# Optimization experiments

Measured on AMD Instinct MI355X. Metric: run time of the kernel, lower is better.

The kernel has to match this reference:

```python
import jax, jax.numpy as jnp
import numpy as np

NUM_EMBEDDINGS = 8192
EMBEDDING_DIM = 256
COMMITMENT_COST = 0.25


def setup_inputs() -> dict:
    key = jax.random.key(0)
    k1, k2 = jax.random.split(key)
    inputs = jax.random.normal(k1, (64, 512, EMBEDDING_DIM), dtype=jnp.float32)
    # nn.Embedding weight initialized uniform(-0.1, 0.1)
    emb_w = jax.random.uniform(k2, (NUM_EMBEDDINGS, EMBEDDING_DIM), dtype=jnp.float32,
                               minval=-0.1, maxval=0.1)
    return {"inputs": inputs, "emb_w": emb_w}


def reference(inputs, emb_w):
    x = jnp.clip(inputs, -1.0, 1.0)
    flat = x.reshape(-1, EMBEDDING_DIM)                      # [N, D]
    distances = (jnp.sum(flat * flat, axis=1, keepdims=True)
                 + jnp.sum(emb_w * emb_w, axis=1)
                 - 2.0 * jnp.einsum('nd,kd->nk', flat, emb_w))
    encoding_indices = jnp.argmin(distances, axis=1)         # [N]
    quantized = emb_w[encoding_indices].reshape(x.shape)     # [B, T, D]
    # loss = mse(stop_grad(q), x) + beta * mse(q, stop_grad(x))
    loss = (jnp.mean((jax.lax.stop_gradient(quantized) - x) ** 2)
            + COMMITMENT_COST * jnp.mean((quantized - jax.lax.stop_gradient(x)) ** 2))
    # straight-through estimator
    quantized_st = x + jax.lax.stop_gradient(quantized - x)
    return (quantized_st, loss)
```

## Files before the change

### kernel.cpp

```cpp
#include <hip/hip_runtime.h>


#define D        256
#define KCODES   8192
#define NROWS    32768
#define MB       64
#define SLOTS    128
#define THREADS  512
#define CAP      32
#define MARGIN   0.03f
#define BIAS     32.0f
#define NOUT     8388608

typedef _Float16 h8_t __attribute__((ext_vector_type(8)));
typedef float    f4_t __attribute__((ext_vector_type(4)));

__device__ __forceinline__ float clipf(float v) { return fminf(1.0f, fmaxf(-1.0f, v)); }

#define DPP_ROR(x, n) __int_as_float(__builtin_amdgcn_update_dpp( \
    0, __float_as_int(x), 0x120 + (n), 0xF, 0xF, true))
__device__ __forceinline__ float maxrow16(float x) {
  x = fmaxf(x, DPP_ROR(x, 1));
  x = fmaxf(x, DPP_ROR(x, 2));
  x = fmaxf(x, DPP_ROR(x, 4));
  x = fmaxf(x, DPP_ROR(x, 8));
  return x;
}

__global__ void vq_packsetup(const float* __restrict__ emb, _Float16* __restrict__ femb,
                             float* __restrict__ senp, float* __restrict__ ekkb,
                             float* __restrict__ lossacc) {
  const int t = blockIdx.x;
  if (t == 0 && threadIdx.x == 0) lossacc[0] = 0.0f;
  #pragma unroll
  for (int j = 0; j < 4; ++j) {
    int g = t * 1024 + j * 256 + threadIdx.x;
    int ch = g >> 9, u = g & 511;
    int kc = u >> 6, ln = u & 63;
    int code = ch * 16 + (ln & 15);
    int k0 = kc * 32 + (ln >> 4) * 8;
    const float* sp = emb + (size_t)code * D + k0;
    f4_t v0 = *(const f4_t*)sp, v1 = *(const f4_t*)(sp + 4);
    h8_t h;
    h[0] = (_Float16)v0[0]; h[1] = (_Float16)v0[1];
    h[2] = (_Float16)v0[2]; h[3] = (_Float16)v0[3];
    h[4] = (_Float16)v1[0]; h[5] = (_Float16)v1[1];
    h[6] = (_Float16)v1[2]; h[7] = (_Float16)v1[3];
    *(h8_t*)(femb + (size_t)g * 8) = h;
  }
  const int lane = threadIdx.x & 63;
  const int w    = threadIdx.x >> 6;
  const int jdx  = lane & 15, hf = jdx >> 3, jj = jdx & 7;
  #pragma unroll
  for (int cc = 0; cc < 2; ++cc) {
    int k = t * 32 + w * 8 + cc * 4 + (lane >> 4);
    const float* base = emb + (size_t)k * D + hf * 128 + jj;
    float v = base[0];
    float r = v * v;
    #pragma unroll
    for (int m = 1; m < 16; ++m) { v = base[8 * m]; r += v * v; }
    r += __shfl_xor(r, 1, 64);
    r += __shfl_xor(r, 2, 64);
    r += __shfl_xor(r, 4, 64);
    r += __shfl_xor(r, 8, 64);
    if (jdx == 0) { senp[k] = r; ekkb[k] = 0.5f * r - BIAS; }
  }
}

__global__ void __launch_bounds__(THREADS, 4)
vq_score(const float* __restrict__ xin, const _Float16* __restrict__ femb,
         const float* __restrict__ ekkb, int* __restrict__ gcnt,
         unsigned short* __restrict__ gcand) {
  __shared__ alignas(16) char Astage[32768];
  __shared__ int rowmaxI[MB];
  __shared__ int cnt[MB];
  __shared__ unsigned short cand[MB][CAP];

  const int tid  = threadIdx.x;
  const int lane = tid & 63;
  const int wid  = tid >> 6;
  const int l15  = lane & 15;
  const int quad = lane >> 4;
  const int rw   = wid >> 2;
  const int cq   = wid & 3;
  const int r0   = blockIdx.x * MB;

  for (int i = tid; i < MB; i += THREADS) { rowmaxI[i] = 0; cnt[i] = 0; }

  #pragma unroll
  for (int j = 0; j < 4; ++j) {
    int c = j * THREADS + tid;
    int ms = c >> 9, kc = (c >> 6) & 7, ln = c & 63;
    int row = ms * 16 + (ln & 15);
    int k0 = kc * 32 + (ln >> 4) * 8;
    const float* ap = xin + (size_t)(r0 + row) * D + k0;
    f4_t v0 = *(const f4_t*)ap, v1 = *(const f4_t*)(ap + 4);
    h8_t h;
    h[0] = (_Float16)clipf(v0[0]); h[1] = (_Float16)clipf(v0[1]);
    h[2] = (_Float16)clipf(v0[2]); h[3] = (_Float16)clipf(v0[3]);
    h[4] = (_Float16)clipf(v1[0]); h[5] = (_Float16)clipf(v1[1]);
    h[6] = (_Float16)clipf(v1[2]); h[7] = (_Float16)clipf(v1[3]);
    *(h8_t*)(Astage + (size_t)c * 16) = h;
  }
  __syncthreads();

  h8_t afrag[2][8];
  #pragma unroll
  for (int m = 0; m < 2; ++m)
    #pragma unroll
    for (int kc = 0; kc < 8; ++kc)
      afrag[m][kc] = *(const h8_t*)(Astage +
          (size_t)(((rw * 2 + m) * 512 + kc * 64 + lane) * 16));

  float Gm[2];
  Gm[0] = -1e30f; Gm[1] = -1e30f;

  h8_t bcur[8]; float ekcur;
  {
    const _Float16* bb = femb + (size_t)cq * 4096 + lane * 8;
    #pragma unroll
    for (int kc = 0; kc < 8; ++kc) bcur[kc] = *(const h8_t*)(bb + kc * 512);
    ekcur = ekkb[cq * 16 + l15];
  }

  for (int s = 0; s < SLOTS; ++s) {
    f4_t acc[2];
    #pragma unroll
    for (int m = 0; m < 2; ++m) { f4_t z = {0.f, 0.f, 0.f, 0.f}; acc[m] = z; }
    #pragma unroll
    for (int kc = 0; kc < 8; ++kc)
      #pragma unroll
      for (int m = 0; m < 2; ++m)
        acc[m] = __builtin_amdgcn_mfma_f32_16x16x32_f16(afrag[m][kc], bcur[kc], acc[m], 0, 0, 0);

    const int sn = (s + 1 < SLOTS) ? s + 1 : s;
    float eknext;
    {
      const _Float16* bb = femb + (size_t)(sn * 4 + cq) * 4096 + lane * 8;
      #pragma unroll
      for (int kc = 0; kc < 8; ++kc) bcur[kc] = *(const h8_t*)(bb + kc * 512);
      eknext = ekkb[(sn * 4 + cq) * 16 + l15];
    }

    const int ch = s * 4 + cq;
    #pragma unroll
    for (int m = 0; m < 2; ++m) {
      float ts[4];
      #pragma unroll
      for (int r = 0; r < 4; ++r) ts[r] = acc[m][r] - ekcur;
      float tmx = fmaxf(fmaxf(ts[0], ts[1]), fmaxf(ts[2], ts[3]));
      if (__any(tmx > Gm[m])) {
        float cmin = 1e30f;
        #pragma unroll
        for (int r = 0; r < 4; ++r) {
          int row_ = rw * 32 + m * 16 + quad * 4 + r;
          float mm = maxrow16(ts[r]);
          if (l15 == 0) atomicMax(&rowmaxI[row_], __float_as_int(mm));
          float cut = __int_as_float(rowmaxI[row_]) - MARGIN;
          cmin = fminf(cmin, cut);
          if (ts[r] >= cut) {
            int sidx = atomicAdd(&cnt[row_], 1);
            if (sidx < CAP) cand[row_][sidx] = (unsigned short)(ch * 16 + l15);
          }
        }
        Gm[m] = cmin;
      }
    }
    ekcur = eknext;
    if ((s & 31) == 31) __syncthreads();
  }
  __syncthreads();

  for (int i = tid; i < MB; i += THREADS) {
    int c = cnt[i];
    gcnt[r0 + i] = c > CAP ? CAP : c;
  }
  const unsigned int* cu = (const unsigned int*)cand;
  unsigned int* gu = (unsigned int*)gcand + (size_t)r0 * (CAP / 2);
  for (int i = tid; i < MB * (CAP / 2); i += THREADS) gu[i] = cu[i];
}

__global__ void __launch_bounds__(512)
vq_rescore(const float* __restrict__ xin, const float* __restrict__ emb,
           const float* __restrict__ senp, const int* __restrict__ gcnt,
           const unsigned short* __restrict__ gcand, float* __restrict__ out,
           float* __restrict__ lossacc) {
  __shared__ float xrow[8][D];
  __shared__ float rpart[8][16];
  __shared__ float blksum;
  const int tid  = threadIdx.x;
  const int lane = tid & 63;
  const int wid  = tid >> 6;
  const int g    = lane >> 3;
  const int e    = lane & 7;
  const int r0   = blockIdx.x * 64;
  if (tid == 0) blksum = 0.0f;
  __syncthreads();

  const int lane4 = lane * 4;
  for (int rr = 0; rr < 8; ++rr) {
    const int row = wid + rr * 8;
    f4_t xv = *(const f4_t*)(xin + (size_t)(r0 + row) * D + lane4);
    xv[0] = clipf(xv[0]); xv[1] = clipf(xv[1]); xv[2] = clipf(xv[2]); xv[3] = clipf(xv[3]);
    *(f4_t*)&xrow[wid][lane4] = xv;
    __builtin_amdgcn_wave_barrier();
    if (lane < 16) {
      const int hf = lane >> 3, jj = lane & 7;
      const float* base = &xrow[wid][hf * 128 + jj];
      float v = base[0];
      float rs = v * v;
      #pragma unroll
      for (int m = 1; m < 16; ++m) { v = base[8 * m]; rs += v * v; }
      rpart[wid][lane] = rs;
    }
    __builtin_amdgcn_wave_barrier();
    float p[16];
    #pragma unroll
    for (int j = 0; j < 16; ++j) p[j] = rpart[wid][j];
    float h0 = ((p[0] + p[1]) + (p[2] + p[3])) + ((p[4] + p[5]) + (p[6] + p[7]));
    float h1 = ((p[8] + p[9]) + (p[10] + p[11])) + ((p[12] + p[13]) + (p[14] + p[15]));
    float sx = h0 + h1;

    f4_t xo[8];
    #pragma unroll
    for (int u = 0; u < 8; ++u) xo[u] = *(const f4_t*)&xrow[wid][e * 32 + u * 4];

    const int nc = gcnt[r0 + row];
    const unsigned short* cl = gcand + (size_t)(r0 + row) * CAP;
    float bd = INFINITY; int bk = 0x7fffffff;
    for (int bi = 0; bi < (nc + 7) >> 3; ++bi) {
      int ci = bi * 8 + g;
      bool valid = ci < nc;
      int k = valid ? cl[ci] : 0;
      const float* ep = emb + (size_t)k * D + e * 32;
      double dd = 0.0;
      #pragma unroll
      for (int u = 0; u < 8; ++u) {
        f4_t ev = *(const f4_t*)(ep + u * 4);
        dd += (double)xo[u][0] * (double)ev[0] + (double)xo[u][1] * (double)ev[1]
            + (double)xo[u][2] * (double)ev[2] + (double)xo[u][3] * (double)ev[3];
      }
      dd += __shfl_xor(dd, 1, 64);
      dd += __shfl_xor(dd, 2, 64);
      dd += __shfl_xor(dd, 4, 64);
      float T1 = sx + senp[k];
      float T2 = (float)(2.0 * dd);
      float d  = valid ? (T1 - T2) : INFINITY;
      int   kk = valid ? k : 0x7fffffff;
      if (d < bd || (d == bd && kk < bk)) { bd = d; bk = kk; }
    }
    #pragma unroll
    for (int off = 8; off < 64; off <<= 1) {
      float od = __shfl_xor(bd, off, 64);
      int   ok = __shfl_xor(bk, off, 64);
      if (od < bd || (od == bd && ok < bk)) { bd = od; bk = ok; }
    }

    f4_t ev = *(const f4_t*)(emb + (size_t)bk * D + lane4);
    *(f4_t*)(out + (size_t)(r0 + row) * D + lane4) = ev;
    float ls = 0.0f;
    #pragma unroll
    for (int i = 0; i < 4; ++i) { float df = ev[i] - xv[i]; ls += df * df; }
    #pragma unroll
    for (int off = 1; off < 64; off <<= 1) ls += __shfl_xor(ls, off, 64);
    if (lane == 0) atomicAdd(&blksum, ls);
  }
  __syncthreads();
  if (tid == 0) atomicAdd(lossacc, blksum);
}

__global__ void vq_fin(const float* __restrict__ lossacc, float* __restrict__ out) {
  out[NOUT] = 1.25f * lossacc[0] / 8388608.0f;
}

extern "C" void kernel_launch(void* const* d_in, const int* in_sizes, int n_in,
                              void* d_out, int out_size, void* d_ws, size_t ws_size,
                              hipStream_t stream) {
  const float* xin = (const float*)d_in[0];
  const float* emb = (const float*)d_in[1];
  float* out = (float*)d_out;
  _Float16* femb = (_Float16*)d_ws;
  float* F       = (float*)d_ws + 1048576;
  float* senp    = F;
  float* ekkb    = F + 8192;
  float* lossacc = F + 16384;
  int*   gcnt    = (int*)(F + 16640);
  unsigned short* gcand = (unsigned short*)(F + 16640 + 32768);
  vq_packsetup<<<dim3(256), dim3(256), 0, stream>>>(emb, femb, senp, ekkb, lossacc);
  vq_score<<<dim3(NROWS / MB), dim3(THREADS), 0, stream>>>(xin, femb, ekkb, gcnt, gcand);
  vq_rescore<<<dim3(NROWS / 64), dim3(512), 0, stream>>>(xin, emb, senp, gcnt, gcand, out, lossacc);
  vq_fin<<<dim3(1), dim3(1), 0, stream>>>(lossacc, out);
}
```

Measured before the change: 300.7 us.

## Stream codebook tiles into double-buffered LDS with direct global-to-LDS loads

The score kernel now stages each slot's 32KB fp16 codebook tile into a double-buffered LDS region using global_load_lds, instead of every wave loading its B fragments straight from global memory into registers. All four column-quarter waves sharing a row group then read B from LDS, which cuts redundant global/L2 traffic and register pressure, at the cost of a block-wide barrier every slot and 64KB of LDS, which may lower occupancy. Separately, the pack-setup kernel is launched with 1024 blocks doing one conversion each rather than 256 blocks doing four, to expose more parallelism.

```diff
diff --git a/kernel.cpp b/kernel.cpp
--- a/kernel.cpp
+++ b/kernel.cpp
@@ -17,6 +17,12 @@
 
 __device__ __forceinline__ float clipf(float v) { return fminf(1.0f, fmaxf(-1.0f, v)); }
 
+__device__ __forceinline__ void gload_lds16(const void* g, void* l) {
+  __builtin_amdgcn_global_load_lds(
+      (const __attribute__((address_space(1))) unsigned int*)g,
+      (__attribute__((address_space(3))) unsigned int*)l, 16, 0, 0);
+}
+
 #define DPP_ROR(x, n) __int_as_float(__builtin_amdgcn_update_dpp( \
     0, __float_as_int(x), 0x120 + (n), 0xF, 0xF, true))
 __device__ __forceinline__ float maxrow16(float x) {
@@ -32,9 +38,8 @@
                              float* __restrict__ lossacc) {
   const int t = blockIdx.x;
   if (t == 0 && threadIdx.x == 0) lossacc[0] = 0.0f;
-  #pragma unroll
-  for (int j = 0; j < 4; ++j) {
-    int g = t * 1024 + j * 256 + threadIdx.x;
+  {
+    int g = t * 256 + threadIdx.x;
     int ch = g >> 9, u = g & 511;
     int kc = u >> 6, ln = u & 63;
     int code = ch * 16 + (ln & 15);
@@ -48,22 +53,24 @@
     h[6] = (_Float16)v1[2]; h[7] = (_Float16)v1[3];
     *(h8_t*)(femb + (size_t)g * 8) = h;
   }
-  const int lane = threadIdx.x & 63;
-  const int w    = threadIdx.x >> 6;
-  const int jdx  = lane & 15, hf = jdx >> 3, jj = jdx & 7;
-  #pragma unroll
-  for (int cc = 0; cc < 2; ++cc) {
-    int k = t * 32 + w * 8 + cc * 4 + (lane >> 4);
-    const float* base = emb + (size_t)k * D + hf * 128 + jj;
-    float v = base[0];
-    float r = v * v;
-    #pragma unroll
-    for (int m = 1; m < 16; ++m) { v = base[8 * m]; r += v * v; }
-    r += __shfl_xor(r, 1, 64);
-    r += __shfl_xor(r, 2, 64);
-    r += __shfl_xor(r, 4, 64);
-    r += __shfl_xor(r, 8, 64);
-    if (jdx == 0) { senp[k] = r; ekkb[k] = 0.5f * r - BIAS; }
+  if (t < 256) {
+    const int lane = threadIdx.x & 63;
+    const int w    = threadIdx.x >> 6;
+    const int jdx  = lane & 15, hf = jdx >> 3, jj = jdx & 7;
+    #pragma unroll
+    for (int cc = 0; cc < 2; ++cc) {
+      int k = t * 32 + w * 8 + cc * 4 + (lane >> 4);
+      const float* base = emb + (size_t)k * D + hf * 128 + jj;
+      float v = base[0];
+      float r = v * v;
+      #pragma unroll
+      for (int m = 1; m < 16; ++m) { v = base[8 * m]; r += v * v; }
+      r += __shfl_xor(r, 1, 64);
+      r += __shfl_xor(r, 2, 64);
+      r += __shfl_xor(r, 4, 64);
+      r += __shfl_xor(r, 8, 64);
+      if (jdx == 0) { senp[k] = r; ekkb[k] = 0.5f * r - BIAS; }
+    }
   }
 }
 
@@ -71,7 +78,7 @@
 vq_score(const float* __restrict__ xin, const _Float16* __restrict__ femb,
          const float* __restrict__ ekkb, int* __restrict__ gcnt,
          unsigned short* __restrict__ gcand) {
-  __shared__ alignas(16) char Astage[32768];
+  __shared__ alignas(16) char Bbuf[2][32768];
   __shared__ int rowmaxI[MB];
   __shared__ int cnt[MB];
   __shared__ unsigned short cand[MB][CAP];
@@ -87,20 +94,23 @@
 
   for (int i = tid; i < MB; i += THREADS) { rowmaxI[i] = 0; cnt[i] = 0; }
 
-  #pragma unroll
-  for (int j = 0; j < 4; ++j) {
-    int c = j * THREADS + tid;
-    int ms = c >> 9, kc = (c >> 6) & 7, ln = c & 63;
-    int row = ms * 16 + (ln & 15);
-    int k0 = kc * 32 + (ln >> 4) * 8;
-    const float* ap = xin + (size_t)(r0 + row) * D + k0;
-    f4_t v0 = *(const f4_t*)ap, v1 = *(const f4_t*)(ap + 4);
-    h8_t h;
-    h[0] = (_Float16)clipf(v0[0]); h[1] = (_Float16)clipf(v0[1]);
-    h[2] = (_Float16)clipf(v0[2]); h[3] = (_Float16)clipf(v0[3]);
-    h[4] = (_Float16)clipf(v1[0]); h[5] = (_Float16)clipf(v1[1]);
-    h[6] = (_Float16)clipf(v1[2]); h[7] = (_Float16)clipf(v1[3]);
-    *(h8_t*)(Astage + (size_t)c * 16) = h;
+  {
+    char* Astage = &Bbuf[0][0];
+    #pragma unroll
+    for (int j = 0; j < 4; ++j) {
+      int c = j * THREADS + tid;
+      int ms = c >> 9, kc = (c >> 6) & 7, ln = c & 63;
+      int row = ms * 16 + (ln & 15);
+      int k0 = kc * 32 + (ln >> 4) * 8;
+      const float* ap = xin + (size_t)(r0 + row) * D + k0;
+      f4_t v0 = *(const f4_t*)ap, v1 = *(const f4_t*)(ap + 4);
+      h8_t h;
+      h[0] = (_Float16)clipf(v0[0]); h[1] = (_Float16)clipf(v0[1]);
+      h[2] = (_Float16)clipf(v0[2]); h[3] = (_Float16)clipf(v0[3]);
+      h[4] = (_Float16)clipf(v1[0]); h[5] = (_Float16)clipf(v1[1]);
+      h[6] = (_Float16)clipf(v1[2]); h[7] = (_Float16)clipf(v1[3]);
+      *(h8_t*)(Astage + (size_t)c * 16) = h;
+    }
   }
   __syncthreads();
 
@@ -109,21 +119,38 @@
   for (int m = 0; m < 2; ++m)
     #pragma unroll
     for (int kc = 0; kc < 8; ++kc)
-      afrag[m][kc] = *(const h8_t*)(Astage +
+      afrag[m][kc] = *(const h8_t*)(&Bbuf[0][0] +
           (size_t)(((rw * 2 + m) * 512 + kc * 64 + lane) * 16));
-
+  __syncthreads();
+
+  const char* fb = (const char*)femb;
+  #pragma unroll
+  for (int j = 0; j < 4; ++j) {
+    int off = j * 8192 + wid * 1024 + lane * 16;
+    gload_lds16(fb + off, &Bbuf[0][off]);
+  }
+  float ekcur = ekkb[cq * 16 + l15];
   float Gm[2];
   Gm[0] = -1e30f; Gm[1] = -1e30f;
-
-  h8_t bcur[8]; float ekcur;
-  {
-    const _Float16* bb = femb + (size_t)cq * 4096 + lane * 8;
-    #pragma unroll
-    for (int kc = 0; kc < 8; ++kc) bcur[kc] = *(const h8_t*)(bb + kc * 512);
-    ekcur = ekkb[cq * 16 + l15];
-  }
+  __syncthreads();
 
   for (int s = 0; s < SLOTS; ++s) {
+    const int cur = s & 1;
+    if (s + 1 < SLOTS) {
+      #pragma unroll
+      for (int j = 0; j < 4; ++j) {
+        int off = j * 8192 + wid * 1024 + lane * 16;
+        gload_lds16(fb + (size_t)(s + 1) * 32768 + off, &Bbuf[cur ^ 1][off]);
+      }
+    }
+    const int sn = (s + 1 < SLOTS) ? s + 1 : s;
+    float eknext = ekkb[(sn * 4 + cq) * 16 + l15];
+
+    h8_t bcur[8];
+    #pragma unroll
+    for (int kc = 0; kc < 8; ++kc)
+      bcur[kc] = *(const h8_t*)(&Bbuf[cur][cq * 8192 + kc * 1024 + lane * 16]);
+
     f4_t acc[2];
     #pragma unroll
     for (int m = 0; m < 2; ++m) { f4_t z = {0.f, 0.f, 0.f, 0.f}; acc[m] = z; }
@@ -132,15 +159,6 @@
       #pragma unroll
       for (int m = 0; m < 2; ++m)
         acc[m] = __builtin_amdgcn_mfma_f32_16x16x32_f16(afrag[m][kc], bcur[kc], acc[m], 0, 0, 0);
-
-    const int sn = (s + 1 < SLOTS) ? s + 1 : s;
-    float eknext;
-    {
-      const _Float16* bb = femb + (size_t)(sn * 4 + cq) * 4096 + lane * 8;
-      #pragma unroll
-      for (int kc = 0; kc < 8; ++kc) bcur[kc] = *(const h8_t*)(bb + kc * 512);
-      eknext = ekkb[(sn * 4 + cq) * 16 + l15];
-    }
 
     const int ch = s * 4 + cq;
     #pragma unroll
@@ -167,9 +185,8 @@
       }
     }
     ekcur = eknext;
-    if ((s & 31) == 31) __syncthreads();
-  }
-  __syncthreads();
+    __syncthreads();
+  }
 
   for (int i = tid; i < MB; i += THREADS) {
     int c = cnt[i];
@@ -286,7 +303,7 @@
   float* lossacc = F + 16384;
   int*   gcnt    = (int*)(F + 16640);
   unsigned short* gcand = (unsigned short*)(F + 16640 + 32768);
-  vq_packsetup<<<dim3(256), dim3(256), 0, stream>>>(emb, femb, senp, ekkb, lossacc);
+  vq_packsetup<<<dim3(1024), dim3(256), 0, stream>>>(emb, femb, senp, ekkb, lossacc);
   vq_score<<<dim3(NROWS / MB), dim3(THREADS), 0, stream>>>(xin, femb, ekkb, gcnt, gcand);
   vq_rescore<<<dim3(NROWS / 64), dim3(512), 0, stream>>>(xin, emb, senp, gcnt, gcand, out, lossacc);
   vq_fin<<<dim3(1), dim3(1), 0, stream>>>(lossacc, out);
```

Result: slower. 339.9 us (+13.0%).
